# Kernel tuning notes

Hardware: AMD Instinct MI355X
Metric: run time of the kernel (lower is better)

## Reference

```python
import jax, jax.numpy as jnp
import numpy as np

BZ, P, T, H = 64, 512, 256, 768  # batch, bpe_seq_len, token seq_len, hidden


def setup_inputs() -> dict:
    key = jax.random.key(0)
    rng = np.random.default_rng(0)
    # variable number of tokens per sentence, each token -> 1 or 2 subwords
    tok_counts = rng.integers(200, T + 1, size=BZ)
    lens = rng.integers(1, 3, size=(BZ, T)).astype(np.int32)  # in {1,2}
    lens = np.where(np.arange(T)[None, :] < tok_counts[:, None], lens, 0)
    totals = lens.sum(axis=1)  # <= 512 == P by construction
    bert_mask = (np.arange(P)[None, :] < totals[:, None]).astype(np.int32)
    enc_out = jax.random.normal(key, (BZ, P, H), dtype=jnp.float32)
    return {
        "enc_out": enc_out,
        "bert_mask": jnp.asarray(bert_mask),
        "bert_lens": jnp.asarray(lens),
    }


def reference(enc_out, bert_mask, bert_lens):
    # enc_out: (BZ, P, H) last BERT hidden states (merge='none')
    # bert_mask: (BZ, P) int {0,1}; bert_lens: (BZ, T) subword counts per token
    bz, p_len, h = enc_out.shape
    t_len = bert_lens.shape[1]
    # cumulative subword counts; subword position p belongs to token
    # t = searchsorted(cum[b], p, 'right')  (zero-length tokens are skipped)
    cum = jnp.cumsum(bert_lens, axis=1)                      # (BZ, T)
    pos = jnp.arange(p_len)
    seg = jax.vmap(lambda c: jnp.searchsorted(c, pos, side='right'))(cum)  # (BZ, P)
    valid = bert_mask.astype(bool)
    dummy = bz * t_len  # trash segment for padding subword positions
    seg_global = jnp.where(valid, seg + jnp.arange(bz)[:, None] * t_len, dummy)
    sums = jax.ops.segment_sum(
        enc_out.reshape(-1, h), seg_global.reshape(-1), num_segments=bz * t_len + 1
    )[: bz * t_len]                                          # (BZ*T, H)
    counts = jnp.maximum(bert_lens.reshape(-1, 1), 1).astype(enc_out.dtype)
    out = (sums / counts).reshape(bz, t_len, h)
    # masked_scatter semantics: positions with lens==0 stay zero
    return jnp.where((bert_lens > 0)[..., None], out, jnp.zeros((), enc_out.dtype))
```

## Files before the change

kernel.cpp:

```cpp
#include <hip/hip_runtime.h>

#define BZ 64
#define P  512
#define T  256
#define H  768
#define H4 (H / 4)

__global__ void scan_kernel(const int* __restrict__ lens, int* __restrict__ starts) {
    __shared__ int sm[T];
    const int b = blockIdx.x;
    const int t = threadIdx.x;
    const int v = lens[b * T + t];
    sm[t] = v;
    __syncthreads();
    #pragma unroll
    for (int off = 1; off < T; off <<= 1) {
        const int add = (t >= off) ? sm[t - off] : 0;
        __syncthreads();
        sm[t] += add;
        __syncthreads();
    }
    starts[b * T + t] = sm[t] - v;
}

__global__ void gather_kernel(const float* __restrict__ enc,
                              const int* __restrict__ lens,
                              const int* __restrict__ starts,
                              float* __restrict__ out) {
    const int idx = blockIdx.x * blockDim.x + threadIdx.x;
    const int h4  = idx % H4;
    const int bt  = idx / H4;
    const int b   = bt / T;

    const int len = lens[bt];
    float4 r = make_float4(0.f, 0.f, 0.f, 0.f);
    if (len > 0) {
        const int start = starts[bt];
        const float4* row =
            (const float4*)(enc + ((size_t)b * P + (size_t)start) * H) + h4;
        r = row[0];
        if (len > 1) {
            #pragma unroll 1
            for (int k = 1; k < len; ++k) {
                const float4 r2 = row[(size_t)k * H4];
                r.x += r2.x; r.y += r2.y; r.z += r2.z; r.w += r2.w;
            }
            const float inv = 1.0f / (float)len;
            r.x *= inv; r.y *= inv; r.z *= inv; r.w *= inv;
        }
    }
    ((float4*)out)[idx] = r;
}

extern "C" void kernel_launch(void* const* d_in, const int* in_sizes, int n_in,
                              void* d_out, int out_size, void* d_ws, size_t ws_size,
                              hipStream_t stream) {
    const float* enc   = (const float*)d_in[0];
    const int*   lens  = (const int*)d_in[2];
    float*       out   = (float*)d_out;
    int*         start = (int*)d_ws;

    scan_kernel<<<BZ, T, 0, stream>>>(lens, start);

    const int total4 = BZ * T * H4;
    gather_kernel<<<total4 / 256, 256, 0, stream>>>(enc, lens, start, out);
}
```

Before: 156.9 us.

## Fuse prefix scan into gather kernel with wave-shuffle scan and batched loads

```diff
diff --git a/kernel.cpp b/kernel.cpp
--- a/kernel.cpp
+++ b/kernel.cpp
@@ -5,63 +5,98 @@
 #define T  256
 #define H  768
 #define H4 (H / 4)
+#define THREADS 256
+#define F4PT 4
+#define F4PB (THREADS * F4PT)
+#define OUT4B (T * H4)
+#define CPB (OUT4B / F4PB)
 
-__global__ void scan_kernel(const int* __restrict__ lens, int* __restrict__ starts) {
-    __shared__ int sm[T];
-    const int b = blockIdx.x;
-    const int t = threadIdx.x;
-    const int v = lens[b * T + t];
-    sm[t] = v;
+__global__ __launch_bounds__(THREADS) void fused_kernel(
+    const float* __restrict__ enc,
+    const int* __restrict__ lens,
+    float* __restrict__ out)
+{
+    __shared__ int s_start[T];
+    __shared__ int s_len[T];
+    __shared__ int s_wsum[THREADS / 64];
+
+    const int tid  = threadIdx.x;
+    const int lane = tid & 63;
+    const int wid  = tid >> 6;
+    const int b    = blockIdx.x / CPB;
+    const int c    = blockIdx.x % CPB;
+
+    const int v = lens[b * T + tid];
+    int x = v;
+    #pragma unroll
+    for (int off = 1; off < 64; off <<= 1) {
+        const int y = __shfl_up(x, off, 64);
+        if (lane >= off) x += y;
+    }
+    if (lane == 63) s_wsum[wid] = x;
     __syncthreads();
+    int woff = 0;
     #pragma unroll
-    for (int off = 1; off < T; off <<= 1) {
-        const int add = (t >= off) ? sm[t - off] : 0;
-        __syncthreads();
-        sm[t] += add;
-        __syncthreads();
+    for (int w = 0; w < THREADS / 64; ++w)
+        woff += (w < wid) ? s_wsum[w] : 0;
+    s_start[tid] = x + woff - v;
+    s_len[tid]   = v;
+    __syncthreads();
+
+    const float4* encb = (const float4*)enc + (size_t)b * P * H4;
+    float4*       outb = (float4*)out + (size_t)b * OUT4B;
+    const int base = c * F4PB + tid;
+
+    int           lq[F4PT];
+    const float4* rq[F4PT];
+    float4 r0[F4PT], r1[F4PT];
+
+    #pragma unroll
+    for (int q = 0; q < F4PT; ++q) {
+        const int f4 = base + q * THREADS;
+        const int t  = f4 / H4;
+        const int h4 = f4 - t * H4;
+        lq[q] = s_len[t];
+        rq[q] = encb + (size_t)s_start[t] * H4 + h4;
     }
-    starts[b * T + t] = sm[t] - v;
-}
-
-__global__ void gather_kernel(const float* __restrict__ enc,
-                              const int* __restrict__ lens,
-                              const int* __restrict__ starts,
-                              float* __restrict__ out) {
-    const int idx = blockIdx.x * blockDim.x + threadIdx.x;
-    const int h4  = idx % H4;
-    const int bt  = idx / H4;
-    const int b   = bt / T;
-
-    const int len = lens[bt];
-    float4 r = make_float4(0.f, 0.f, 0.f, 0.f);
-    if (len > 0) {
-        const int start = starts[bt];
-        const float4* row =
-            (const float4*)(enc + ((size_t)b * P + (size_t)start) * H) + h4;
-        r = row[0];
+    #pragma unroll
+    for (int q = 0; q < F4PT; ++q) {
+        r0[q] = (lq[q] > 0) ? rq[q][0]
+                            : make_float4(0.f, 0.f, 0.f, 0.f);
+    }
+    #pragma unroll
+    for (int q = 0; q < F4PT; ++q) {
+        r1[q] = (lq[q] > 1) ? rq[q][H4]
+                            : make_float4(0.f, 0.f, 0.f, 0.f);
+    }
+    #pragma unroll
+    for (int q = 0; q < F4PT; ++q) {
+        float4 r = r0[q];
+        const int len = lq[q];
         if (len > 1) {
-            #pragma unroll 1
-            for (int k = 1; k < len; ++k) {
-                const float4 r2 = row[(size_t)k * H4];
-                r.x += r2.x; r.y += r2.y; r.z += r2.z; r.w += r2.w;
+            r.x += r1[q].x; r.y += r1[q].y; r.z += r1[q].z; r.w += r1[q].w;
+            if (len > 2) {
+                #pragma unroll 1
+                for (int k = 2; k < len; ++k) {
+                    const float4 e = rq[q][(size_t)k * H4];
+                    r.x += e.x; r.y += e.y; r.z += e.z; r.w += e.w;
+                }
             }
             const float inv = 1.0f / (float)len;
             r.x *= inv; r.y *= inv; r.z *= inv; r.w *= inv;
         }
+        outb[base + q * THREADS] = r;
     }
-    ((float4*)out)[idx] = r;
 }
 
 extern "C" void kernel_launch(void* const* d_in, const int* in_sizes, int n_in,
                               void* d_out, int out_size, void* d_ws, size_t ws_size,
-                              hipStream_t stream) {
-    const float* enc   = (const float*)d_in[0];
-    const int*   lens  = (const int*)d_in[2];
-    float*       out   = (float*)d_out;
-    int*         start = (int*)d_ws;
+                              hipStream_t stream)
+{
+    const float* enc  = (const float*)d_in[0];
+    const int*   lens = (const int*)d_in[2];
+    float*       out  = (float*)d_out;
+    (void)d_ws; (void)ws_size; (void)in_sizes; (void)n_in; (void)out_size;
 
-    scan_kernel<<<BZ, T, 0, stream>>>(lens, start);
-
-    const int total4 = BZ * T * H4;
-    gather_kernel<<<total4 / 256, 256, 0, stream>>>(enc, lens, start, out);
+    fused_kernel<<<BZ * CPB, THREADS, 0, stream>>>(enc, lens, out);
 }
```

Result: no change. 156.6 us (-0.2%).
